# Kernel tuning notes

Measured on AMD Instinct MI355X. Metric: run time of the kernel, lower is better.

Reference implementation:

```python
import jax, jax.numpy as jnp
import numpy as np

B, FEW, NSN, NQ, NN = 256, 5, 5, 10, 512
M, D, H, L, NSYM = 200, 100, 450, 2, 70000
BETA, MARGIN = 5.0, 1.0


def _lstm_dir(x, W_ih, W_hh, b_ih, b_hh):
    # x: (T, B, in) -> outputs (T, B, H), final h (B, H). PyTorch gate order i,f,g,o.
    Bn, Hn = x.shape[1], W_hh.shape[1]
    def cell(carry, xt):
        h, c = carry
        g = xt @ W_ih.T + h @ W_hh.T + b_ih + b_hh
        i, f, gg, o = jnp.split(g, 4, axis=-1)
        c = jax.nn.sigmoid(f) * c + jax.nn.sigmoid(i) * jnp.tanh(gg)
        h = jax.nn.sigmoid(o) * jnp.tanh(c)
        return (h, c), h
    z = jnp.zeros((Bn, Hn), x.dtype)
    (hT, _), ys = jax.lax.scan(cell, (z, z), x)
    return ys, hT


def _bidir(x, Wih, Whh, bih, bhh):
    # Wih: (2, 4H, in) stacked [fwd, bwd]
    yf, hf = _lstm_dir(x, Wih[0], Whh[0], bih[0], bhh[0])
    yb, hb = _lstm_dir(x[::-1], Wih[1], Whh[1], bih[1], bhh[1])
    return jnp.concatenate([yf, yb[::-1]], -1), hf, hb


def setup_inputs():
    key = jax.random.key(0)
    ks = jax.random.split(key, 30)
    f32 = jnp.float32
    emb = jax.random.normal(ks[0], (NSYM + 1, D), f32) * 0.1
    emb = emb.at[NSYM].set(0.0)  # padding_idx
    s = 0.05
    inp = dict(
        support=jax.random.normal(ks[1], (B, FEW, 2, D), f32),
        support_negative=jax.random.normal(ks[2], (B, NSN, 2, D), f32),
        query=jax.random.normal(ks[3], (B, NQ, 2, D), f32),
        negative=jax.random.normal(ks[4], (B, NN, 2, D), f32),
        norm_vector=jax.random.normal(ks[5], (B, 1, 1, D), f32),
        left_conn=jax.random.randint(ks[6], (FEW, B, M, 3), 0, NSYM, jnp.int32),
        right_conn=jax.random.randint(ks[7], (FEW, B, M, 3), 0, NSYM, jnp.int32),
        symbol_emb=emb,
        gcn_w=jax.random.normal(ks[8], (D, 2 * D), f32) * s,
        gcn_wb=jnp.zeros((D,), f32),
        gcn_b=jnp.zeros((D,), f32),
        attn_w=jax.random.normal(ks[9], (1, D), f32) * s,
        attn_wb=jnp.zeros((1,), f32),
        gate_w=jax.random.normal(ks[10], (1, D), f32) * s,
        gate_wb=jnp.zeros((1,), f32),
        gate_b=jnp.zeros((1,), f32),
        Wih0=jax.random.normal(ks[11], (2, 4 * H, 2 * D), f32) * s,
        Whh0=jax.random.normal(ks[12], (2, 4 * H, H), f32) * s,
        bih0=jnp.zeros((2, 4 * H), f32),
        bhh0=jnp.zeros((2, 4 * H), f32),
        Wih1=jax.random.normal(ks[13], (2, 4 * H, 2 * H), f32) * s,
        Whh1=jax.random.normal(ks[14], (2, 4 * H, H), f32) * s,
        bih1=jnp.zeros((2, 4 * H), f32),
        bhh1=jnp.zeros((2, 4 * H), f32),
        out_w=jax.random.normal(ks[15], (D, 2 * H * L), f32) * s,
        out_b=jnp.zeros((D,), f32),
    )
    return inp


def reference(support, support_negative, query, negative, norm_vector,
              left_conn, right_conn, symbol_emb,
              gcn_w, gcn_wb, gcn_b, attn_w, attn_wb, gate_w, gate_wb, gate_b,
              Wih0, Whh0, bih0, bhh0, Wih1, Whh1, bih1, bhh1, out_w, out_b):
    few, b, m, _ = left_conn.shape
    d = symbol_emb.shape[1]

    def neighbor_encoder(conn):  # (N, M, 3) -> (N, D); dropout=identity (eval)
        rel_e = symbol_emb[conn[:, :, 1]]            # (N, M, D)
        ent_e = symbol_emb[conn[:, :, 2]]            # (N, M, D)
        self_e = symbol_emb[conn[:, 0, 0]]           # (N, D)
        cat = jnp.concatenate([rel_e, ent_e], -1)    # (N, M, 2D)
        out = jax.nn.leaky_relu(cat @ gcn_w.T + gcn_wb + gcn_b, 0.01)
        attn = jax.nn.softmax(out @ attn_w.T + attn_wb, axis=1)  # (N, M, 1)
        out_attn = jnp.einsum('nmd,nm->nd', out, attn[..., 0])
        gate = jax.nn.sigmoid(out_attn @ gate_w.T + gate_wb + gate_b)  # (N, 1)
        return out_attn * gate + self_e * (1.0 - gate)

    # all (few, left/right) encodings in one fused pass
    conn_all = jnp.stack([left_conn, right_conn], 1).reshape(few * 2 * b, m, 3)
    enc = neighbor_encoder(conn_all).reshape(few, 2, b, d).transpose(2, 0, 1, 3)  # (B, few, 2, D)

    # LSTM_attn relation learner
    x = enc.reshape(b, few, 2 * d).transpose(1, 0, 2)  # (T=few, B, 2D)
    y, h0f, h0b = _bidir(x, Wih0, Whh0, bih0, bhh0)
    y, h1f, h1b = _bidir(y, Wih1, Whh1, bih1, bhh1)
    final = jnp.stack([h0f, h0b, h1f, h1b], 0)         # (2*L, B, H)
    output = y.transpose(1, 0, 2)                       # (B, T, 2H)
    hidden = final.reshape(-1, 2 * H, L)                # faithful to torch .view
    aw = jax.nn.softmax(jnp.einsum('bth,bhl->btl', output, hidden), axis=1)
    context = jnp.einsum('bth,btl->bhl', output, aw).reshape(b, 2 * H * L)
    rel = (context @ out_w.T + out_b).reshape(b, 1, 1, d)

    def split_concat(pos, neg):
        e1 = jnp.concatenate([pos[:, :, 0, :], neg[:, :, 0, :]], 1)[:, :, None, :]
        e2 = jnp.concatenate([pos[:, :, 1, :], neg[:, :, 1, :]], 1)[:, :, None, :]
        return e1, e2

    def emb_learner(h, t, r, norm, pos_num):
        norm = norm[:, :1, :, :]
        h = h - jnp.sum(h * norm, -1, keepdims=True) * norm
        t = t - jnp.sum(t * norm, -1, keepdims=True) * norm
        score = -jnp.linalg.norm(h + r - t, axis=-1)[:, :, 0]
        return score[:, :pos_num], score[:, pos_num:]

    nsn = support_negative.shape[1]
    def inner_loss(rel_):
        rel_s = jnp.broadcast_to(rel_, (b, few + nsn, 1, d))
        e1, e2 = split_concat(support, support_negative)
        p, n = emb_learner(e1, e2, rel_s, norm_vector, few)
        return jnp.mean(jax.nn.relu(MARGIN - (p - n)))

    grad_meta = jax.grad(inner_loss)(rel)
    rel_q = rel - BETA * grad_meta
    norm_q = norm_vector - BETA * grad_meta

    nq, nn = query.shape[1], negative.shape[1]
    e1, e2 = split_concat(query, negative)
    rel_qe = jnp.broadcast_to(rel_q, (b, nq + nn, 1, d))
    p_score, n_score = emb_learner(e1, e2, rel_qe, norm_q, nq)
    return p_score, n_score
```

## Files before the change

### kernel.cpp

```cpp
#include <hip/hip_runtime.h>

typedef unsigned short u16;
typedef unsigned int   u32;
typedef __attribute__((ext_vector_type(8))) short short8;
typedef __attribute__((ext_vector_type(4))) float f32x4;

__device__ __forceinline__ float u2f(u32 u){
  union { u32 i; float f; } v; v.i = u << 16; return v.f;
}
__device__ __forceinline__ u16 f2bu(float f){
  union { float f; u32 i; } v; v.f = f;
  u32 i = v.i;
  i += 0x7fffu + ((i >> 16) & 1u);
  return (u16)(i >> 16);
}
__device__ __forceinline__ float sigm(float x){ return 1.0f/(1.0f + expf(-x)); }
__device__ __forceinline__ float ldf(const void* p, size_t i, int bf){
  return bf ? u2f(((const u16*)p)[i]) : ((const float*)p)[i];
}
__device__ __forceinline__ float wsum(float v){
  #pragma unroll
  for (int off = 32; off > 0; off >>= 1) v += __shfl_xor(v, off, 64);
  return v;
}

__global__ __launch_bounds__(64) void k_detect(const u32* __restrict__ nv,
                                               int* __restrict__ flag)
{
  int i = threadIdx.x;
  u32 w = nv[i];
  u32 e = (w >> 7) & 0xffu;
  bool sane = (e >= 100u && e <= 140u);
  unsigned long long m = __ballot(sane);
  if (i == 0) *flag = (__popcll(m) >= 40) ? 1 : 0;
}

__global__ __launch_bounds__(256) void k_prep(
    const void* __restrict__ gcnw, u16* __restrict__ Wg,
    const void* __restrict__ emb, u16* __restrict__ Eb,
    const int* __restrict__ flag)
{
  const int bf = *flag;
  int idx = blockIdx.x*256 + threadIdx.x;
  if (idx < 25088){
    int r = idx / 224, k = idx - r*224;
    u16 v = 0;
    if (k < 200 && r < 100){
      size_t si = (size_t)r*200 + k;
      v = bf ? ((const u16*)gcnw)[si] : f2bu(((const float*)gcnw)[si]);
    }
    Wg[idx] = v;
    return;
  }
  int e4 = idx - 25088;
  if (e4 >= 1750025) return;
  size_t i = (size_t)e4*4;
  union { u16 q[4]; uint2 d; } o;
  if (bf){
    o.d = *(const uint2*)((const u16*)emb + i);
  } else {
    float4 t = *(const float4*)((const float*)emb + i);
    o.q[0] = f2bu(t.x); o.q[1] = f2bu(t.y);
    o.q[2] = f2bu(t.z); o.q[3] = f2bu(t.w);
  }
  *(uint2*)(Eb + i) = o.d;
}

__device__ __forceinline__ void packg_one(
    const void* __restrict__ src, u16* __restrict__ dst,
    int K, int Kp, int bf, int idx)
{
  const int Kq = Kp >> 2;
  const int per = 1920*Kq;
  int z = idx / per, r = idx - z*per;
  int rp = r / Kq, cq = r - rp*Kq;
  int c0 = cq*4;
  int kblk = rp >> 6, rem = rp & 63, gate = rem >> 4, klo = rem & 15;
  int k = kblk*16 + klo;
  union { u16 q[4]; uint2 d; } o;
  o.q[0] = 0; o.q[1] = 0; o.q[2] = 0; o.q[3] = 0;
  if (k < 450){
    size_t base = ((size_t)z*1800 + (size_t)gate*450 + k)*K;
    #pragma unroll
    for (int e = 0; e < 4; ++e){
      int c = c0 + e;
      if (c < K)
        o.q[e] = bf ? ((const u16*)src)[base+c] : f2bu(((const float*)src)[base+c]);
    }
  }
  *(uint2*)(dst + (size_t)idx*4) = o.d;
}

__global__ __launch_bounds__(256) void k_packL(
    const void* __restrict__ Wih, int Kih, int KpIh, u16* __restrict__ Wp,
    const void* __restrict__ Whh, u16* __restrict__ Whp,
    const void* __restrict__ bih, const void* __restrict__ bhh,
    float* __restrict__ Bp, const int* __restrict__ flag)
{
  const int bf = *flag;
  const int n1 = 2*1920*(KpIh >> 2);
  const int n2 = 2*1920*120;
  int idx = blockIdx.x*256 + threadIdx.x;
  if (idx < n1){ packg_one(Wih, Wp, Kih, KpIh, bf, idx); return; }
  idx -= n1;
  if (idx < n2){ packg_one(Whh, Whp, 450, 480, bf, idx); return; }
  idx -= n2;
  if (idx >= 2*1920) return;
  int z = idx / 1920, rp = idx - z*1920;
  int kblk = rp >> 6, rem = rp & 63, gate = rem >> 4, klo = rem & 15;
  int k = kblk*16 + klo;
  float v = 0.0f;
  if (k < 450){
    size_t si = (size_t)z*1800 + (size_t)gate*450 + k;
    v = ldf(bih, si, bf) + ldf(bhh, si, bf);
  }
  Bp[idx] = v;
}

__global__ __launch_bounds__(512, 4) void k_gcn(
    const int* __restrict__ left, const int* __restrict__ right,
    const void* __restrict__ emb, const u16* __restrict__ Eb,
    const u16* __restrict__ Wg,
    const void* __restrict__ gcnwb, const void* __restrict__ gcnb,
    const void* __restrict__ attnw, const void* __restrict__ attnwb,
    const void* __restrict__ gatew, const void* __restrict__ gatewb,
    const void* __restrict__ gateb,
    const int* __restrict__ flag,
    u16* __restrict__ X0bf)
{
  __shared__ __align__(16) u16 As[208*40];
  __shared__ __align__(16) u16 Bs[112*232];
  __shared__ int c1_s[200], c2_s[200];
  __shared__ float logit_s[208];
  __shared__ float red_s[512];
  __shared__ float attnw_s[112], bias_s[112], gatew_s[112], oa_s[112];

  const int bf  = *flag;
  const int tid = threadIdx.x;
  const int n   = blockIdx.x;
  const int b   = n & 255;
  const int fs  = n >> 8;
  const int s   = fs & 1;
  const int f   = fs >> 1;
  const int* conn = (s == 0 ? left : right) + (size_t)(f*256 + b)*600;

  if (tid < 200){ c1_s[tid] = conn[tid*3+1]; c2_s[tid] = conn[tid*3+2]; }
  if (tid < 112){
    attnw_s[tid] = (tid < 100) ? ldf(attnw, tid, bf) : 0.0f;
    bias_s[tid]  = (tid < 100) ? (ldf(gcnwb, tid, bf) + ldf(gcnb, tid, bf)) : 0.0f;
    gatew_s[tid] = (tid < 100) ? ldf(gatew, tid, bf) : 0.0f;
    oa_s[tid] = 0.0f;
  }
  for (int g = tid; g < 112*28; g += 512){
    int r = g / 28, cc = g - r*28;
    *(short8*)(Bs + r*232 + cc*8) = *(const short8*)(Wg + (size_t)r*224 + cc*8);
  }
  if (s == 1 && tid >= 100 && tid < 124)
    X0bf[((size_t)f*256 + b)*224 + 100 + tid] = 0;
  __syncthreads();

  const int wid  = tid >> 6, lane = tid & 63, ln = lane & 15, quad = lane >> 4;
  const int mt0 = (wid < 5) ? 2*wid : (10 + (wid - 5));
  const int nmt = (wid < 5) ? 2 : 1;

  auto loadA = [&](int kc, uint2* pv){
    #pragma unroll
    for (int it = 0; it < 4; ++it){
      int g = tid + it*512;
      uint2 v; v.x = 0u; v.y = 0u;
      if (g < 1664){
        int r = g >> 3, gi = g & 7, k = kc*32 + gi*4;
        if (r < 200 && k < 200){
          int c  = (k < 100) ? c1_s[r] : c2_s[r];
          int kk = (k < 100) ? k : (k - 100);
          v = *(const uint2*)(Eb + (size_t)c*100 + kk);
        }
      }
      pv[it] = v;
    }
  };

  f32x4 acc[2][7];
  #pragma unroll
  for (int i = 0; i < 2; ++i)
    #pragma unroll
    for (int j = 0; j < 7; ++j) acc[i][j] = (f32x4)0.0f;

  uint2 pv[4];
  loadA(0, pv);

  for (int kc = 0; kc < 7; ++kc){
    const int k0 = kc*32;
    #pragma unroll
    for (int it = 0; it < 4; ++it){
      int g = tid + it*512;
      if (g < 1664){
        int r = g >> 3, gi = g & 7;
        *(uint2*)(As + r*40 + gi*4) = pv[it];
      }
    }
    __syncthreads();
    if (kc < 6) loadA(kc+1, pv);

    #pragma unroll
    for (int mi = 0; mi < 2; ++mi){
      if (mi < nmt){
        short8 afr = *(const short8*)(As + ((mt0+mi)*16 + ln)*40 + quad*8);
        #pragma unroll
        for (int nt = 0; nt < 7; ++nt){
          short8 bfr = *(const short8*)(Bs + (size_t)(nt*16 + ln)*232 + k0 + quad*8);
          acc[mi][nt] = __builtin_amdgcn_mfma_f32_16x16x32_bf16(afr, bfr, acc[mi][nt], 0, 0, 0);
        }
      }
    }
    __syncthreads();
  }

  const float awb = ldf(attnwb, 0, bf);
  #pragma unroll
  for (int mi = 0; mi < 2; ++mi){
    if (mi < nmt){
      #pragma unroll
      for (int rg = 0; rg < 4; ++rg){
        float p = 0.0f;
        #pragma unroll
        for (int nt = 0; nt < 7; ++nt){
          float x = acc[mi][nt][rg] + bias_s[nt*16 + ln];
          x = x > 0.0f ? x : 0.01f*x;
          p += x * attnw_s[nt*16 + ln];
        }
        p += __shfl_xor(p, 1, 64); p += __shfl_xor(p, 2, 64);
        p += __shfl_xor(p, 4, 64); p += __shfl_xor(p, 8, 64);
        int m = (mt0+mi)*16 + quad*4 + rg;
        if (ln == 0 && m < 200) logit_s[m] = p + awb;
      }
    }
  }
  __syncthreads();

  red_s[tid] = (tid < 200) ? logit_s[tid] : -3.0e38f;
  __syncthreads();
  for (int off = 256; off > 0; off >>= 1){
    if (tid < off) red_s[tid] = fmaxf(red_s[tid], red_s[tid+off]);
    __syncthreads();
  }
  float mx = red_s[0];
  __syncthreads();
  float ev = 0.0f;
  if (tid < 200) ev = expf(logit_s[tid] - mx);
  red_s[tid] = ev;
  __syncthreads();
  for (int off = 256; off > 0; off >>= 1){
    if (tid < off) red_s[tid] += red_s[tid+off];
    __syncthreads();
  }
  float S = red_s[0];
  __syncthreads();
  if (tid < 208) logit_s[tid] = (tid < 200) ? ev*(1.0f/S) : 0.0f;
  __syncthreads();

  float at[2][4];
  #pragma unroll
  for (int mi = 0; mi < 2; ++mi)
    #pragma unroll
    for (int rg = 0; rg < 4; ++rg)
      at[mi][rg] = (mi < nmt) ? logit_s[(mt0+mi)*16 + quad*4 + rg] : 0.0f;

  #pragma unroll
  for (int nt = 0; nt < 7; ++nt){
    float p = 0.0f;
    #pragma unroll
    for (int mi = 0; mi < 2; ++mi){
      if (mi < nmt){
        #pragma unroll
        for (int rg = 0; rg < 4; ++rg){
          float x = acc[mi][nt][rg] + bias_s[nt*16 + ln];
          x = x > 0.0f ? x : 0.01f*x;
          p += x * at[mi][rg];
        }
      }
    }
    p += __shfl_xor(p, 16, 64); p += __shfl_xor(p, 32, 64);
    if (quad == 0) atomicAdd(&oa_s[nt*16 + ln], p);
  }
  __syncthreads();

  red_s[tid] = (tid < 100) ? oa_s[tid]*gatew_s[tid] : 0.0f;
  __syncthreads();
  for (int off = 256; off > 0; off >>= 1){
    if (tid < off) red_s[tid] += red_s[tid+off];
    __syncthreads();
  }
  float gate = sigm(red_s[0] + ldf(gatewb, 0, bf) + ldf(gateb, 0, bf));
  if (tid < 100){
    int c0 = conn[0];
    float self = ldf(emb, (size_t)c0*100 + tid, bf);
    X0bf[((size_t)f*256 + b)*224 + s*100 + tid] = f2bu(oa_s[tid]*gate + self*(1.0f - gate));
  }
}

__global__ __launch_bounds__(256) void k_mgemm(
    const u16* __restrict__ A, int lda, size_t Astride,
    const u16* __restrict__ B, int ldb, size_t Bstride,
    const float* __restrict__ bsum,
    u16* __restrict__ out, size_t Ostride,
    int N, int KC)
{
  __shared__ __align__(16) u16 As[128*40];
  __shared__ __align__(16) u16 Bs[128*40];
  const int tid = threadIdx.x;
  const int z  = blockIdx.z;
  const int nb = blockIdx.x, mb = blockIdx.y;
  const u16* Az = A + (size_t)z*Astride;
  const u16* Bz = B + (size_t)z*Bstride;

  const int wid = tid >> 6, lane = tid & 63, ln = lane & 15, quad = lane >> 4;
  const int wm = wid >> 1, wn = wid & 1;

  f32x4 acc[4][4];
  #pragma unroll
  for (int i = 0; i < 4; ++i)
    #pragma unroll
    for (int j = 0; j < 4; ++j) acc[i][j] = (f32x4)0.0f;

  const int srow = tid >> 1;
  const int koff = (tid & 1)*16;
  const int rowA = mb*128 + srow;
  const int rowB = nb*128 + srow;

  for (int kc = 0; kc < KC; ++kc){
    const int k0 = kc*32 + koff;
    const u16* ap = Az + (size_t)rowA*lda + k0;
    const u16* bp = Bz + (size_t)rowB*ldb + k0;
    short8 av0 = *(const short8*)(ap);
    short8 av1 = *(const short8*)(ap + 8);
    short8 bv0 = *(const short8*)(bp);
    short8 bv1 = *(const short8*)(bp + 8);
    *(short8*)(As + srow*40 + koff)     = av0;
    *(short8*)(As + srow*40 + koff + 8) = av1;
    *(short8*)(Bs + srow*40 + koff)     = bv0;
    *(short8*)(Bs + srow*40 + koff + 8) = bv1;
    __syncthreads();
    short8 af[4], bfr[4];
    #pragma unroll
    for (int i = 0; i < 4; ++i)
      af[i] = *(const short8*)(As + (wm*64 + i*16 + ln)*40 + quad*8);
    #pragma unroll
    for (int j = 0; j < 4; ++j)
      bfr[j] = *(const short8*)(Bs + (wn*64 + j*16 + ln)*40 + quad*8);
    #pragma unroll
    for (int i = 0; i < 4; ++i)
      #pragma unroll
      for (int j = 0; j < 4; ++j)
        acc[i][j] = __builtin_amdgcn_mfma_f32_16x16x32_bf16(af[i], bfr[j], acc[i][j], 0, 0, 0);
    __syncthreads();
  }

  #pragma unroll
  for (int j = 0; j < 4; ++j){
    int col = nb*128 + wn*64 + j*16 + ln;
    float bias = bsum ? bsum[(size_t)z*1920 + col] : 0.0f;
    #pragma unroll
    for (int i = 0; i < 4; ++i){
      #pragma unroll
      for (int rg = 0; rg < 4; ++rg){
        int row = mb*128 + wm*64 + i*16 + quad*4 + rg;
        out[(size_t)z*Ostride + (size_t)row*N + col] = f2bu(acc[i][j][rg] + bias);
      }
    }
  }
}

__global__ __launch_bounds__(64) void k_hstep(
    const u16* __restrict__ Hin, const u16* __restrict__ Whp,
    const u16* __restrict__ Gb, float* __restrict__ HC,
    u16* __restrict__ Hout, u16* __restrict__ Ybf, float* __restrict__ Yf,
    float* __restrict__ HF, int s, int layer, int first)
{
  const int lane = threadIdx.x;
  const int ln = lane & 15, quad = lane >> 4;
  const int kb = blockIdx.x;
  const int mb = blockIdx.y;
  const int z  = blockIdx.z;

  f32x4 acc[4];
  #pragma unroll
  for (int j = 0; j < 4; ++j) acc[j] = (f32x4)0.0f;

  if (!first){
    const u16* Az = Hin + ((size_t)z*256 + mb*16)*480;
    const u16* Bz = Whp + (size_t)z*1920*480 + (size_t)kb*64*480;
    #pragma unroll
    for (int kc = 0; kc < 15; ++kc){
      const int k0 = kc*32 + quad*8;
      short8 afr = *(const short8*)(Az + (size_t)ln*480 + k0);
      #pragma unroll
      for (int j = 0; j < 4; ++j){
        short8 bfr = *(const short8*)(Bz + (size_t)(j*16 + ln)*480 + k0);
        acc[j] = __builtin_amdgcn_mfma_f32_16x16x32_bf16(afr, bfr, acc[j], 0, 0, 0);
      }
    }
  }

  const int k = kb*16 + ln;
  const int t = z ? (4 - s) : s;
  if (k < 450){
    const u16* Gz = Gb + (size_t)z*2457600 + (size_t)t*256*1920;
    #pragma unroll
    for (int rg = 0; rg < 4; ++rg){
      int b = mb*16 + quad*4 + rg;
      const u16* grow = Gz + (size_t)b*1920 + kb*64 + ln;
      float gi = acc[0][rg] + u2f(grow[0]);
      float gf = acc[1][rg] + u2f(grow[16]);
      float gg = acc[2][rg] + u2f(grow[32]);
      float go = acc[3][rg] + u2f(grow[48]);
      float* cp = HC + ((size_t)(2+z)*256 + b)*450 + k;
      float cprv = first ? 0.0f : *cp;
      float c = sigm(gf)*cprv + sigm(gi)*tanhf(gg);
      float h = sigm(go)*tanhf(c);
      *cp = c;
      Hout[((size_t)z*256 + b)*480 + k] = f2bu(h);
      if (Ybf) Ybf[((size_t)t*256 + b)*928 + z*450 + k] = f2bu(h);
      else     Yf [((size_t)t*256 + b)*900 + z*450 + k] = h;
      HF[((size_t)(layer*2+z)*256 + b)*450 + k] = h;
    }
  } else {
    #pragma unroll
    for (int rg = 0; rg < 4; ++rg){
      int b = mb*16 + quad*4 + rg;
      Hout[((size_t)z*256 + b)*480 + k] = 0;
      if (z == 1 && Ybf && k < 478)
        Ybf[((size_t)t*256 + b)*928 + 450 + k] = 0;
    }
  }
}

__global__ __launch_bounds__(256) void k_attn(
    const float* __restrict__ Y1, const float* __restrict__ HF,
    float* __restrict__ CTX)
{
  __shared__ float red2[40];
  __shared__ float aw[10];
  int b = blockIdx.x, tid = threadIdx.x;
  int wid = tid >> 6, lane = tid & 63;
  for (int p = 0; p < 10; ++p){
    int t = p >> 1, l = p & 1;
    float a = 0.0f;
    for (int h = tid; h < 900; h += 256)
      a += Y1[((size_t)t*256 + b)*900 + h] * HF[(size_t)b*1800 + h*2 + l];
    a = wsum(a);
    if (lane == 0) red2[p*4 + wid] = a;
  }
  __syncthreads();
  if (tid < 2){
    int l = tid;
    float sc[5];
    float mxv = -3.0e38f;
    for (int t = 0; t < 5; ++t){
      int p = t*2 + l;
      sc[t] = red2[p*4] + red2[p*4+1] + red2[p*4+2] + red2[p*4+3];
      mxv = fmaxf(mxv, sc[t]);
    }
    float e[5], sum = 0.0f;
    for (int t = 0; t < 5; ++t){ e[t] = expf(sc[t]-mxv); sum += e[t]; }
    for (int t = 0; t < 5; ++t) aw[t*2+l] = e[t]/sum;
  }
  __syncthreads();
  for (int h = tid; h < 900; h += 256){
    float v0 = 0.0f, v1 = 0.0f;
    for (int t = 0; t < 5; ++t){
      float y = Y1[((size_t)t*256 + b)*900 + h];
      v0 += y*aw[t*2+0]; v1 += y*aw[t*2+1];
    }
    CTX[(size_t)b*1800 + h*2 + 0] = v0;
    CTX[(size_t)b*1800 + h*2 + 1] = v1;
  }
}

__global__ __launch_bounds__(256) void k_gemm(
    const float* __restrict__ A, const void* __restrict__ W, size_t wEl,
    const void* __restrict__ b1, const void* __restrict__ b2, size_t bEl,
    const int* __restrict__ flag,
    float* __restrict__ out, int K, int C)
{
  extern __shared__ float a_s[];
  const int bf = *flag;
  const int tid = threadIdx.x;
  const int r = blockIdx.y;
  const float* a = A + (size_t)r*K;
  for (int k = tid; k < K; k += 256) a_s[k] = a[k];
  __syncthreads();
  const int j = blockIdx.x*256 + tid;
  if (j >= C) return;
  float acc = 0.0f;
  if (b1) acc += ldf(b1, bEl + j, bf);
  if (b2) acc += ldf(b2, bEl + j, bf);
  if (bf){
    const u16* w = (const u16*)W + wEl + (size_t)j*K;
    for (int k = 0; k < K; k += 4){
      uint2 wv = *(const uint2*)(w + k);
      acc += a_s[k]   * u2f(wv.x & 0xffffu);
      acc += a_s[k+1] * u2f(wv.x >> 16);
      acc += a_s[k+2] * u2f(wv.y & 0xffffu);
      acc += a_s[k+3] * u2f(wv.y >> 16);
    }
  } else {
    const float* w = (const float*)W + wEl + (size_t)j*K;
    for (int k = 0; k < K; k += 4){
      float4 wv = *(const float4*)(w + k);
      acc += a_s[k]*wv.x + a_s[k+1]*wv.y + a_s[k+2]*wv.z + a_s[k+3]*wv.w;
    }
  }
  out[(size_t)r*C + j] = acc;
}

__global__ __launch_bounds__(64) void k_grad(
    const void* __restrict__ sup, const void* __restrict__ supn,
    const void* __restrict__ normv, const float* __restrict__ REL,
    const int* __restrict__ flag,
    float* __restrict__ RELQ, float* __restrict__ NORMQ)
{
  const int bf = *flag;
  const int b = blockIdx.x, lane = threadIdx.x;
  const int d0 = lane, d1 = lane + 64;
  const bool a1 = (d1 < 100);
  float nv0 = ldf(normv, (size_t)b*100 + d0, bf);
  float nv1 = a1 ? ldf(normv, (size_t)b*100 + d1, bf) : 0.0f;
  float rl0 = REL[(size_t)b*100 + d0];
  float rl1 = a1 ? REL[(size_t)b*100 + d1] : 0.0f;
  float acc0 = 0.0f, acc1 = 0.0f;
  for (int j = 0; j < 5; ++j){
    size_t base = (size_t)(b*5+j)*200;
    float h10 = ldf(sup,  base + d0, bf);
    float t10 = ldf(sup,  base + 100 + d0, bf);
    float h20 = ldf(supn, base + d0, bf);
    float t20 = ldf(supn, base + 100 + d0, bf);
    float h11 = a1 ? ldf(sup,  base + d1, bf) : 0.0f;
    float t11 = a1 ? ldf(sup,  base + 100 + d1, bf) : 0.0f;
    float h21 = a1 ? ldf(supn, base + d1, bf) : 0.0f;
    float t21 = a1 ? ldf(supn, base + 100 + d1, bf) : 0.0f;
    float hd1 = wsum(h10*nv0 + h11*nv1);
    float td1 = wsum(t10*nv0 + t11*nv1);
    float hd2 = wsum(h20*nv0 + h21*nv1);
    float td2 = wsum(t20*nv0 + t21*nv1);
    float upd0 = (h10 - hd1*nv0) + rl0 - (t10 - td1*nv0);
    float upd1 = (h11 - hd1*nv1) + rl1 - (t11 - td1*nv1);
    float und0 = (h20 - hd2*nv0) + rl0 - (t20 - td2*nv0);
    float und1 = (h21 - hd2*nv1) + rl1 - (t21 - td2*nv1);
    if (!a1){ upd1 = 0.0f; und1 = 0.0f; }
    float np2 = wsum(upd0*upd0 + upd1*upd1);
    float nn2 = wsum(und0*und0 + und1*und1);
    float p = -sqrtf(np2), nsc = -sqrtf(nn2);
    if (1.0f - (p - nsc) > 0.0f){
      float ip = 1.0f/sqrtf(np2), in = 1.0f/sqrtf(nn2);
      acc0 += upd0*ip - und0*in;
      acc1 += upd1*ip - und1*in;
    }
  }
  float g0 = acc0 * (1.0f/1280.0f);
  RELQ [(size_t)b*100 + d0] = rl0 - 5.0f*g0;
  NORMQ[(size_t)b*100 + d0] = nv0 - 5.0f*g0;
  if (a1){
    float g1 = acc1 * (1.0f/1280.0f);
    RELQ [(size_t)b*100 + d1] = rl1 - 5.0f*g1;
    NORMQ[(size_t)b*100 + d1] = nv1 - 5.0f*g1;
  }
}

__global__ __launch_bounds__(256) void k_score(
    const void* __restrict__ query, const void* __restrict__ neg,
    const float* __restrict__ RELQ, const float* __restrict__ NORMQ,
    const int* __restrict__ flag, void* __restrict__ out)
{
  __shared__ __align__(16) float nq[104], rq[104];
  const int bf = *flag;
  const int b = blockIdx.x, tid = threadIdx.x;
  if (tid < 100){ nq[tid] = NORMQ[b*100+tid]; rq[tid] = RELQ[b*100+tid]; }
  __syncthreads();
  const int wid = tid >> 6, lane = tid & 63;
  const bool lo = (lane < 25);
  const bool hi = (lane >= 32 && lane < 57);
  const int d0 = lo ? lane*4 : (hi ? (lane-32)*4 : 0);
  float4 w4 = make_float4(0.0f,0.0f,0.0f,0.0f);
  float4 r4 = make_float4(0.0f,0.0f,0.0f,0.0f);
  if (lo || hi) w4 = *(const float4*)(nq + d0);
  if (lo)       r4 = *(const float4*)(rq + d0);

  for (int qi = blockIdx.y*4 + wid; qi < 522; qi += 32){
    const void* src = (qi < 10) ? query : neg;
    size_t row = (qi < 10) ? ((size_t)b*10 + qi) : ((size_t)b*512 + qi - 10);
    size_t base = row*200 + (hi ? 100 : 0) + d0;
    float4 v = make_float4(0.0f,0.0f,0.0f,0.0f);
    if (lo || hi){
      if (bf){
        uint2 u = *(const uint2*)((const u16*)src + base);
        v.x = u2f(u.x & 0xffffu); v.y = u2f(u.x >> 16);
        v.z = u2f(u.y & 0xffffu); v.w = u2f(u.y >> 16);
      } else {
        v = *(const float4*)((const float*)src + base);
      }
    }
    float pr = v.x*w4.x + v.y*w4.y + v.z*w4.z + v.w*w4.w;
    #pragma unroll
    for (int off = 16; off > 0; off >>= 1) pr += __shfl_xor(pr, off, 32);
    float tdv = __shfl(pr, lane + 32, 64);
    float4 t4;
    t4.x = __shfl(v.x, lane + 32, 64);
    t4.y = __shfl(v.y, lane + 32, 64);
    t4.z = __shfl(v.z, lane + 32, 64);
    t4.w = __shfl(v.w, lane + 32, 64);
    float s2 = 0.0f;
    if (lo){
      float ux = (v.x - pr*w4.x) + r4.x - (t4.x - tdv*w4.x);
      float uy = (v.y - pr*w4.y) + r4.y - (t4.y - tdv*w4.y);
      float uz = (v.z - pr*w4.z) + r4.z - (t4.z - tdv*w4.z);
      float uw = (v.w - pr*w4.w) + r4.w - (t4.w - tdv*w4.w);
      s2 = ux*ux + uy*uy + uz*uz + uw*uw;
    }
    #pragma unroll
    for (int off = 16; off > 0; off >>= 1) s2 += __shfl_xor(s2, off, 32);
    if (lane == 0){
      float sc = -sqrtf(s2);
      size_t oi = (qi < 10) ? ((size_t)b*10 + qi) : (2560 + (size_t)b*512 + (qi - 10));
      if (bf) ((u16*)out)[oi] = f2bu(sc);
      else    ((float*)out)[oi] = sc;
    }
  }
}

extern "C" void kernel_launch(void* const* d_in, const int* in_sizes, int n_in,
                              void* d_out, int out_size, void* d_ws, size_t ws_size,
                              hipStream_t stream)
{
  const void* support = d_in[0];
  const void* supneg  = d_in[1];
  const void* query   = d_in[2];
  const void* negat   = d_in[3];
  const void* normv   = d_in[4];
  const int* left     = (const int*)d_in[5];
  const int* right    = (const int*)d_in[6];
  const void* emb     = d_in[7];
  const void* gcnw    = d_in[8];
  const void* gcnwb   = d_in[9];
  const void* gcnb    = d_in[10];
  const void* attnw   = d_in[11];
  const void* attnwb  = d_in[12];
  const void* gatew   = d_in[13];
  const void* gatewb  = d_in[14];
  const void* gateb   = d_in[15];
  const void* Wih0    = d_in[16];
  const void* Whh0    = d_in[17];
  const void* bih0    = d_in[18];
  const void* bhh0    = d_in[19];
  const void* Wih1    = d_in[20];
  const void* Whh1    = d_in[21];
  const void* bih1    = d_in[22];
  const void* bhh1    = d_in[23];
  const void* outw    = d_in[24];
  const void* outb    = d_in[25];

  int*   dflag = (int*)d_ws;
  float* fws   = (float*)d_ws + 16;
  float* Y1   = fws;
  float* HF   = Y1 + 1152000;
  float* HC   = HF + 460800;
  float* CTX  = HC + 460800;
  float* RELb = CTX + 460800;
  float* RELQ = RELb + 25600;
  float* NORMQ= RELQ + 25600;
  float* Bp   = NORMQ + 25600;
  float* fend = Bp + 3840;
  u16* Gb   = (u16*)fend;
  u16* X0bf = Gb + 4915200;
  u16* Y0bf = X0bf + 286720;
  u16* Hbf  = Y0bf + 1187840;
  u16* Wg   = Hbf + 491520;
  u16* Eb   = Wg + 25088;
  u16* Wp   = Eb;
  u16* Whp  = Eb + 3563520;

  k_detect<<<1, 64, 0, stream>>>((const u32*)normv, dflag);

  k_prep<<<(25088+1750025+255)/256, 256, 0, stream>>>(gcnw, Wg, emb, Eb, dflag);
  k_gcn<<<2560, 512, 0, stream>>>(left, right, emb, Eb, Wg, gcnwb, gcnb,
                                  attnw, attnwb, gatew, gatewb, gateb,
                                  dflag, X0bf);

  u16* Hpar0 = Hbf;
  u16* Hpar1 = Hbf + 245760;

  k_packL<<<(2*1920*(224/4) + 2*1920*120 + 3840 + 255)/256, 256, 0, stream>>>(
      Wih0, 200, 224, Wp, Whh0, Whp, bih0, bhh0, Bp, dflag);
  k_mgemm<<<dim3(15,10,2), 256, 0, stream>>>(
      X0bf, 224, 0, Wp, 224, (size_t)1920*224,
      Bp, Gb, 2457600, 1920, 7);
  {
    u16* hc = Hpar0; u16* hn = Hpar1;
    for (int s = 0; s < 5; ++s){
      k_hstep<<<dim3(30,16,2), 64, 0, stream>>>(hc, Whp, Gb, HC, hn,
                                                Y0bf, nullptr, HF, s, 0, s==0);
      u16* tmp = hc; hc = hn; hn = tmp;
    }
  }

  k_packL<<<(2*1920*(928/4) + 2*1920*120 + 3840 + 255)/256, 256, 0, stream>>>(
      Wih1, 900, 928, Wp, Whh1, Whp, bih1, bhh1, Bp, dflag);
  k_mgemm<<<dim3(15,10,2), 256, 0, stream>>>(
      Y0bf, 928, 0, Wp, 928, (size_t)1920*928,
      Bp, Gb, 2457600, 1920, 29);
  {
    u16* hc = Hpar0; u16* hn = Hpar1;
    for (int s = 0; s < 5; ++s){
      k_hstep<<<dim3(30,16,2), 64, 0, stream>>>(hc, Whp, Gb, HC, hn,
                                                nullptr, Y1, HF, s, 1, s==0);
      u16* tmp = hc; hc = hn; hn = tmp;
    }
  }

  k_attn<<<256, 256, 0, stream>>>(Y1, HF, CTX);
  k_gemm<<<dim3(1,256), 256, 1800*4, stream>>>(CTX, outw, 0, outb, nullptr, 0,
                                               dflag, RELb, 1800, 100);
  k_grad<<<256, 64, 0, stream>>>(support, supneg, normv, RELb, dflag, RELQ, NORMQ);
  k_score<<<dim3(256,8), 256, 0, stream>>>(query, negat, RELQ, NORMQ, dflag, d_out);
}
```

Baseline: 644.0 us.

## Pad embedding rows to 112 for 16-byte gathers; double hstep batch tile

The bf16 embedding table is now written with rows padded to 112 elements, so the GCN A-tile gather can use 16-byte loads instead of 8-byte loads. The row boundary at k=96..103 is handled by splitting into two 8-byte loads. Separately, the LSTM recurrent step kernel now processes 32 batch rows per block instead of 16, so each B-fragment load feeds two MFMAs and half as many blocks are launched. The cost is a larger padded table, more accumulator registers, and less grid parallelism in the recurrent step.

```diff
diff --git a/kernel.cpp b/kernel.cpp
--- a/kernel.cpp
+++ b/kernel.cpp
@@ -53,17 +53,19 @@
     return;
   }
   int e4 = idx - 25088;
-  if (e4 >= 1750025) return;
-  size_t i = (size_t)e4*4;
+  if (e4 >= 70001*28) return;
+  int row = e4 / 28, cq = e4 - row*28;
+  int c0 = cq*4;
   union { u16 q[4]; uint2 d; } o;
-  if (bf){
-    o.d = *(const uint2*)((const u16*)emb + i);
-  } else {
-    float4 t = *(const float4*)((const float*)emb + i);
-    o.q[0] = f2bu(t.x); o.q[1] = f2bu(t.y);
-    o.q[2] = f2bu(t.z); o.q[3] = f2bu(t.w);
-  }
-  *(uint2*)(Eb + i) = o.d;
+  o.q[0] = 0; o.q[1] = 0; o.q[2] = 0; o.q[3] = 0;
+  size_t sbase = (size_t)row*100;
+  #pragma unroll
+  for (int e = 0; e < 4; ++e){
+    int c = c0 + e;
+    if (c < 100)
+      o.q[e] = bf ? ((const u16*)emb)[sbase+c] : f2bu(((const float*)emb)[sbase+c]);
+  }
+  *(uint2*)(Eb + (size_t)row*112 + c0) = o.d;
 }
 
 __device__ __forceinline__ void packg_one(
@@ -163,17 +165,24 @@
   const int mt0 = (wid < 5) ? 2*wid : (10 + (wid - 5));
   const int nmt = (wid < 5) ? 2 : 1;
 
-  auto loadA = [&](int kc, uint2* pv){
-    #pragma unroll
-    for (int it = 0; it < 4; ++it){
+  auto loadA = [&](int kc, uint4* pv){
+    #pragma unroll
+    for (int it = 0; it < 2; ++it){
       int g = tid + it*512;
-      uint2 v; v.x = 0u; v.y = 0u;
-      if (g < 1664){
-        int r = g >> 3, gi = g & 7, k = kc*32 + gi*4;
+      uint4 v; v.x = 0u; v.y = 0u; v.z = 0u; v.w = 0u;
+      if (g < 832){
+        int r = g >> 2, gi = g & 3, k = kc*32 + gi*8;
         if (r < 200 && k < 200){
-          int c  = (k < 100) ? c1_s[r] : c2_s[r];
-          int kk = (k < 100) ? k : (k - 100);
-          v = *(const uint2*)(Eb + (size_t)c*100 + kk);
+          int c1 = c1_s[r], c2 = c2_s[r];
+          if (k + 8 <= 100){
+            v = *(const uint4*)(Eb + (size_t)c1*112 + k);
+          } else if (k >= 100){
+            v = *(const uint4*)(Eb + (size_t)c2*112 + (k-100));
+          } else {
+            uint2 lo = *(const uint2*)(Eb + (size_t)c1*112 + 96);
+            uint2 hi = *(const uint2*)(Eb + (size_t)c2*112);
+            v.x = lo.x; v.y = lo.y; v.z = hi.x; v.w = hi.y;
+          }
         }
       }
       pv[it] = v;
@@ -186,17 +195,17 @@
     #pragma unroll
     for (int j = 0; j < 7; ++j) acc[i][j] = (f32x4)0.0f;
 
-  uint2 pv[4];
+  uint4 pv[2];
   loadA(0, pv);
 
   for (int kc = 0; kc < 7; ++kc){
     const int k0 = kc*32;
     #pragma unroll
-    for (int it = 0; it < 4; ++it){
+    for (int it = 0; it < 2; ++it){
       int g = tid + it*512;
-      if (g < 1664){
-        int r = g >> 3, gi = g & 7;
-        *(uint2*)(As + r*40 + gi*4) = pv[it];
+      if (g < 832){
+        int r = g >> 2, gi = g & 3;
+        *(uint4*)(As + r*40 + gi*8) = pv[it];
       }
     }
     __syncthreads();
@@ -383,21 +392,25 @@
   const int mb = blockIdx.y;
   const int z  = blockIdx.z;
 
-  f32x4 acc[4];
-  #pragma unroll
-  for (int j = 0; j < 4; ++j) acc[j] = (f32x4)0.0f;
+  f32x4 acc[2][4];
+  #pragma unroll
+  for (int i = 0; i < 2; ++i)
+    #pragma unroll
+    for (int j = 0; j < 4; ++j) acc[i][j] = (f32x4)0.0f;
 
   if (!first){
-    const u16* Az = Hin + ((size_t)z*256 + mb*16)*480;
+    const u16* Az = Hin + ((size_t)z*256 + mb*32)*480;
     const u16* Bz = Whp + (size_t)z*1920*480 + (size_t)kb*64*480;
     #pragma unroll
     for (int kc = 0; kc < 15; ++kc){
       const int k0 = kc*32 + quad*8;
-      short8 afr = *(const short8*)(Az + (size_t)ln*480 + k0);
+      short8 a0 = *(const short8*)(Az + (size_t)ln*480 + k0);
+      short8 a1 = *(const short8*)(Az + (size_t)(16 + ln)*480 + k0);
       #pragma unroll
       for (int j = 0; j < 4; ++j){
         short8 bfr = *(const short8*)(Bz + (size_t)(j*16 + ln)*480 + k0);
-        acc[j] = __builtin_amdgcn_mfma_f32_16x16x32_bf16(afr, bfr, acc[j], 0, 0, 0);
+        acc[0][j] = __builtin_amdgcn_mfma_f32_16x16x32_bf16(a0, bfr, acc[0][j], 0, 0, 0);
+        acc[1][j] = __builtin_amdgcn_mfma_f32_16x16x32_bf16(a1, bfr, acc[1][j], 0, 0, 0);
       }
     }
   }
@@ -407,30 +420,36 @@
   if (k < 450){
     const u16* Gz = Gb + (size_t)z*2457600 + (size_t)t*256*1920;
     #pragma unroll
-    for (int rg = 0; rg < 4; ++rg){
-      int b = mb*16 + quad*4 + rg;
-      const u16* grow = Gz + (size_t)b*1920 + kb*64 + ln;
-      float gi = acc[0][rg] + u2f(grow[0]);
-      float gf = acc[1][rg] + u2f(grow[16]);
-      float gg = acc[2][rg] + u2f(grow[32]);
-      float go = acc[3][rg] + u2f(grow[48]);
-      float* cp = HC + ((size_t)(2+z)*256 + b)*450 + k;
-      float cprv = first ? 0.0f : *cp;
-      float c = sigm(gf)*cprv + sigm(gi)*tanhf(gg);
-      float h = sigm(go)*tanhf(c);
-      *cp = c;
-      Hout[((size_t)z*256 + b)*480 + k] = f2bu(h);
-      if (Ybf) Ybf[((size_t)t*256 + b)*928 + z*450 + k] = f2bu(h);
-      else     Yf [((size_t)t*256 + b)*900 + z*450 + k] = h;
-      HF[((size_t)(layer*2+z)*256 + b)*450 + k] = h;
+    for (int i = 0; i < 2; ++i){
+      #pragma unroll
+      for (int rg = 0; rg < 4; ++rg){
+        int b = mb*32 + i*16 + quad*4 + rg;
+        const u16* grow = Gz + (size_t)b*1920 + kb*64 + ln;
+        float gi = acc[i][0][rg] + u2f(grow[0]);
+        float gf = acc[i][1][rg] + u2f(grow[16]);
+        float gg = acc[i][2][rg] + u2f(grow[32]);
+        float go = acc[i][3][rg] + u2f(grow[48]);
+        float* cp = HC + ((size_t)(2+z)*256 + b)*450 + k;
+        float cprv = first ? 0.0f : *cp;
+        float c = sigm(gf)*cprv + sigm(gi)*tanhf(gg);
+        float h = sigm(go)*tanhf(c);
+        *cp = c;
+        Hout[((size_t)z*256 + b)*480 + k] = f2bu(h);
+        if (Ybf) Ybf[((size_t)t*256 + b)*928 + z*450 + k] = f2bu(h);
+        else     Yf [((size_t)t*256 + b)*900 + z*450 + k] = h;
+        HF[((size_t)(layer*2+z)*256 + b)*450 + k] = h;
+      }
     }
   } else {
     #pragma unroll
-    for (int rg = 0; rg < 4; ++rg){
-      int b = mb*16 + quad*4 + rg;
-      Hout[((size_t)z*256 + b)*480 + k] = 0;
-      if (z == 1 && Ybf && k < 478)
-        Ybf[((size_t)t*256 + b)*928 + 450 + k] = 0;
+    for (int i = 0; i < 2; ++i){
+      #pragma unroll
+      for (int rg = 0; rg < 4; ++rg){
+        int b = mb*32 + i*16 + quad*4 + rg;
+        Hout[((size_t)z*256 + b)*480 + k] = 0;
+        if (z == 1 && Ybf && k < 478)
+          Ybf[((size_t)t*256 + b)*928 + 450 + k] = 0;
+      }
     }
   }
 }
@@ -681,7 +700,7 @@
 
   k_detect<<<1, 64, 0, stream>>>((const u32*)normv, dflag);
 
-  k_prep<<<(25088+1750025+255)/256, 256, 0, stream>>>(gcnw, Wg, emb, Eb, dflag);
+  k_prep<<<(25088 + 70001*28 + 255)/256, 256, 0, stream>>>(gcnw, Wg, emb, Eb, dflag);
   k_gcn<<<2560, 512, 0, stream>>>(left, right, emb, Eb, Wg, gcnwb, gcnb,
                                   attnw, attnwb, gatew, gatewb, gateb,
                                   dflag, X0bf);
@@ -697,8 +716,8 @@
   {
     u16* hc = Hpar0; u16* hn = Hpar1;
     for (int s = 0; s < 5; ++s){
-      k_hstep<<<dim3(30,16,2), 64, 0, stream>>>(hc, Whp, Gb, HC, hn,
-                                                Y0bf, nullptr, HF, s, 0, s==0);
+      k_hstep<<<dim3(30,8,2), 64, 0, stream>>>(hc, Whp, Gb, HC, hn,
+                                               Y0bf, nullptr, HF, s, 0, s==0);
       u16* tmp = hc; hc = hn; hn = tmp;
     }
   }
@@ -711,8 +730,8 @@
   {
     u16* hc = Hpar0; u16* hn = Hpar1;
     for (int s = 0; s < 5; ++s){
-      k_hstep<<<dim3(30,16,2), 64, 0, stream>>>(hc, Whp, Gb, HC, hn,
-                                                nullptr, Y1, HF, s, 1, s==0);
+      k_hstep<<<dim3(30,8,2), 64, 0, stream>>>(hc, Whp, Gb, HC, hn,
+                                               nullptr, Y1, HF, s, 1, s==0);
       u16* tmp = hc; hc = hn; hn = tmp;
     }
   }
```

Result: slower. 677.9 us (+5.3%).
